# Performance work log

Measured on AMD Instinct MI355X. Metric: run time of the kernel, lower is better.

Reference implementation:

```python
import jax, jax.numpy as jnp
import numpy as np

B, IN_CHS, P = 512, 200, 19
CF, TF, K, D, NC = 64, 32, 48, 32, 16
BN_EPS = 1e-5


def _conv(x, w, b=None, dil=1):
    y = jax.lax.conv_general_dilated(x, w, (1, 1), 'VALID',
                                     rhs_dilation=(dil, dil),
                                     dimension_numbers=('NCHW', 'OIHW', 'NCHW'))
    if b is not None:
        y = y + b[None, :, None, None]
    return y


def _upsample_bilinear_ac(x, oh, ow):
    # bilinear with align_corners=True (torch UpsamplingBilinear2d)
    N, C, H, W = x.shape
    ys = jnp.linspace(0.0, H - 1.0, oh)
    xs = jnp.linspace(0.0, W - 1.0, ow)
    y0 = jnp.floor(ys).astype(jnp.int32)
    y1 = jnp.minimum(y0 + 1, H - 1)
    x0 = jnp.floor(xs).astype(jnp.int32)
    x1 = jnp.minimum(x0 + 1, W - 1)
    wy = (ys - y0.astype(ys.dtype))[None, None, :, None]
    wx = (xs - x0.astype(xs.dtype))[None, None, None, :]
    rows = x[:, :, y0, :] * (1.0 - wy) + x[:, :, y1, :] * wy
    return rows[:, :, :, x0] * (1.0 - wx) + rows[:, :, :, x1] * wx


def setup_inputs() -> dict:
    key = jax.random.key(0)
    ks = jax.random.split(key, 24)
    std1 = 1.0 / np.sqrt(K * D)
    inp = {
        'x': jax.random.normal(ks[0], (B, IN_CHS, P, P), jnp.float32),
        'w0': jax.random.normal(ks[1], (CF, IN_CHS, 3, 3), jnp.float32) * 0.02,
        'b0': jnp.zeros((CF,), jnp.float32),
        'w1': jax.random.normal(ks[2], (CF, CF, 3, 3), jnp.float32) * 0.05,
        'b1': jnp.zeros((CF,), jnp.float32),
        'w2': jax.random.normal(ks[3], (CF, CF, 3, 3), jnp.float32) * 0.05,
        'b2': jnp.zeros((CF,), jnp.float32),
        'wa': jax.random.normal(ks[4], (TF, CF, 1, 1), jnp.float32) * 0.08,
        'wb': jax.random.normal(ks[5], (TF, CF, 1, 1), jnp.float32) * 0.08,
        'wg': jax.random.normal(ks[6], (TF, CF, 1, 1), jnp.float32) * 0.08,
        'wd': jax.random.normal(ks[7], (CF, TF, 1, 1), jnp.float32) * 0.08,
        'wenc': jax.random.normal(ks[8], (D, CF, 1, 1), jnp.float32) * 0.08,
        'codewords': jax.random.uniform(ks[9], (K, D), jnp.float32, -std1, std1),
        'scale': jax.random.uniform(ks[10], (K,), jnp.float32, -1.0, 0.0),
        'w_att': jax.random.normal(ks[11], (CF, D), jnp.float32) * 0.1,
        'b_att': jnp.zeros((CF,), jnp.float32),
        'bn_g': jnp.ones((K,), jnp.float32),
        'bn_b': jnp.zeros((K,), jnp.float32),
        'w_d1': jax.random.normal(ks[12], (256, 3 * CF * P * P), jnp.float32) * 0.004,
        'b_d1': jnp.zeros((256,), jnp.float32),
        'w_d2': jax.random.normal(ks[13], (128, 256), jnp.float32) * 0.06,
        'b_d2': jnp.zeros((128,), jnp.float32),
        'w_d3': jax.random.normal(ks[14], (NC, 128), jnp.float32) * 0.09,
        'b_d3': jnp.zeros((NC,), jnp.float32),
    }
    return inp


def reference(x, w0, b0, w1, b1, w2, b2, wa, wb, wg, wd, wenc,
              codewords, scale, w_att, b_att, bn_g, bn_b,
              w_d1, b_d1, w_d2, b_d2, w_d3, b_d3):
    relu = jax.nn.relu
    Hin, Win = x.shape[2], x.shape[3]
    c1 = relu(_conv(x, w0, b0, 1))        # (b, CF, 17, 17)
    c2 = relu(_conv(c1, w1, b1, 2))       # (b, CF, 13, 13)
    xx = relu(_conv(c2, w2, b2, 3))       # (b, CF, 7, 7)
    n, c, h, w = xx.shape
    hw = h * w
    # non-local block; alpha view(n,-1,TF) is a RAW reshape in torch (not a transpose)
    alpha = _conv(xx, wa).reshape(n, hw, TF)
    beta = _conv(xx, wb).reshape(n, TF, hw)
    gam = relu(_conv(xx, wg)).reshape(n, TF, hw)
    ctx = jnp.matmul(alpha, beta)                 # (n, hw, hw)
    ctx = jax.nn.softmax(ctx, axis=0)             # torch F.softmax default dim for 3D tensor is 0
    ctx = jnp.matmul(gam, ctx).reshape(n, TF, h, w)
    ctx = _upsample_bilinear_ac(ctx, h, w)        # same-size -> identity, kept for fidelity
    xx = relu(_conv(ctx, wd)) + xx
    # soft VQ encoding
    Z = relu(_conv(xx, wenc)).reshape(n, D, hw).transpose(0, 2, 1)   # (b, hw, D)
    dist = scale * (jnp.sum(Z * Z, -1, keepdims=True)
                    + jnp.sum(codewords * codewords, -1)[None, None, :]
                    - 2.0 * jnp.einsum('bnd,kd->bnk', Z, codewords))  # (b, hw, K)
    A = jax.nn.softmax(dist, axis=2)
    # E[b,k,d] = sum_n A[b,n,k] * (Z[b,n,d] - C[k,d])
    E = jnp.einsum('bnk,bnd->bkd', A, Z) - A.sum(1)[:, :, None] * codewords[None]
    # BatchNorm1d(K) in training mode: stats over (batch, D) per code k
    mu = E.mean(axis=(0, 2), keepdims=True)
    var = E.var(axis=(0, 2), keepdims=True)
    En = relu((E - mu) / jnp.sqrt(var + BN_EPS) * bn_g[None, :, None] + bn_b[None, :, None])
    E_sum = En.sum(1)                              # (b, D)
    gate = jax.nn.sigmoid(E_sum @ w_att.T + b_att)  # (b, CF)
    xx = xx + xx * gate[:, :, None, None]
    ctx3 = _upsample_bilinear_ac(xx, Hin, Win)
    c2u = _upsample_bilinear_ac(c2, Hin, Win)
    c1u = _upsample_bilinear_ac(c1, Hin, Win)
    feat = jnp.concatenate((c1u, c2u, ctx3), axis=1).reshape(n, -1)  # (b, 69312)
    h1 = relu(feat @ w_d1.T + b_d1)
    h2 = relu(h1 @ w_d2.T + b_d2)
    return h2 @ w_d3.T + b_d3
```

## Files before the change

### kernel.cpp

```cpp
#include <hip/hip_runtime.h>
#include <math.h>


typedef __attribute__((ext_vector_type(8))) short short8v;
typedef __attribute__((ext_vector_type(4))) float f32x4;

#define OFF_WE1H  188928u
#define OFF_WE1L  2556416u
#define OFF_WE2H  4923904u
#define OFF_WE2L  6308352u
#define OFF_WE3H  7692800u
#define OFF_WE3L  8094208u
#define OFF_C1    8495616u
#define OFF_C2    17965568u
#define OFF_XX1   23503360u
#define OFF_ALPHA 25108992u
#define OFF_BETA  25911808u
#define OFF_GAM   26714624u
#define OFF_CTX   27517440u
#define OFF_CTX2  28746752u
#define OFF_XX2   29549568u
#define OFF_Z     31155200u
#define OFF_A     31958016u
#define OFF_E     33162240u
#define OFF_BNS   33948672u
#define OFF_XX3   33948768u
#define OFF_H1    35554400u
#define OFF_H2    35685472u

#define OFF_H1P   OFF_ALPHA

#define OFF_WH    OFF_ALPHA
#define OFF_WL    (OFF_ALPHA + 64512u)
#define OFF_W1H   (OFF_ALPHA + 129024u)
#define OFF_W1L   (OFF_W1H + 18432u)
#define OFF_W2H   (OFF_W1L + 18432u)
#define OFF_W2L   (OFF_W2H + 18432u)

__device__ __forceinline__ unsigned bf16_rne_bits(float v) {
    unsigned u = __float_as_uint(v);
    return (u + 0x7FFFu + ((u >> 16) & 1u)) >> 16;
}

__global__ __launch_bounds__(256) void sac_wsplit(const float* __restrict__ w0,
                                                  unsigned short* __restrict__ WH,
                                                  unsigned short* __restrict__ WL) {
    int idx = blockIdx.x * 256 + threadIdx.x;
    if (idx >= 129024) return;
    int ic = idx % 224;
    int c  = (idx / 224) % 64;
    int s  = idx / (224 * 64);
    int ky = s / 3, kx = s % 3;
    float v = 0.f;
    if (ic < 200) v = w0[((c * 200 + ic) * 3 + ky) * 3 + kx];
    unsigned hb = bf16_rne_bits(v);
    float hf = __uint_as_float(hb << 16);
    unsigned lb = bf16_rne_bits(v - hf);
    WH[idx] = (unsigned short)hb;
    WL[idx] = (unsigned short)lb;
}

__global__ __launch_bounds__(256) void sac_wsplit64(const float* __restrict__ wsrc,
                                                    unsigned short* __restrict__ WHo,
                                                    unsigned short* __restrict__ WLo) {
    int idx = blockIdx.x * 256 + threadIdx.x;
    if (idx >= 36864) return;
    int ic = idx & 63;
    int c  = (idx >> 6) & 63;
    int s  = idx >> 12;
    int ky = s / 3, kx = s - ky * 3;
    float v = wsrc[((c * 64 + ic) * 3 + ky) * 3 + kx];
    unsigned hb = bf16_rne_bits(v);
    float hf = __uint_as_float(hb << 16);
    unsigned lb = bf16_rne_bits(v - hf);
    WHo[idx] = (unsigned short)hb;
    WLo[idx] = (unsigned short)lb;
}

__global__ __launch_bounds__(256) void sac_upA(const float* __restrict__ w_d1,
                                               float* __restrict__ tmp, int S, int co) {
    int idx = blockIdx.x * 256 + threadIdx.x;
    int total = 256 * 64 * 19 * S;
    if (idx >= total) return;
    int xp = idx % S;
    int j  = (idx / S) % 19;
    int c  = (idx / (S * 19)) % 64;
    int o  = idx / (S * 19 * 64);
    const float* wrow = w_d1 + (size_t)o * 69312 + (size_t)(co + c) * 361 + j * 19;
    float ratio = (float)(S - 1) / 18.0f;
    float s = 0.f;
    for (int i = 0; i < 19; ++i) {
        float xs = i * ratio;
        int x0 = (int)floorf(xs);
        float wx = xs - (float)x0;
        int x1 = x0 + 1; if (x1 > S - 1) x1 = S - 1;
        float cf = (xp == x0 ? 1.f - wx : 0.f) + (xp == x1 ? wx : 0.f);
        s += cf * wrow[i];
    }
    tmp[idx] = s;
}
__global__ __launch_bounds__(256) void sac_upB_bf16(const float* __restrict__ tmp,
                                                    unsigned short* __restrict__ WEH,
                                                    unsigned short* __restrict__ WEL, int S) {
    int idx = blockIdx.x * 256 + threadIdx.x;
    int total = 256 * 64 * S * S;
    if (idx >= total) return;
    int xp = idx % S;
    int yp = (idx / S) % S;
    int c  = (idx / (S * S)) % 64;
    int o  = idx / (S * S * 64);
    const float* tp = tmp + (((size_t)o * 64 + c) * 19) * S + xp;
    float ratio = (float)(S - 1) / 18.0f;
    float s = 0.f;
    for (int j = 0; j < 19; ++j) {
        float ys = j * ratio;
        int y0 = (int)floorf(ys);
        float wy = ys - (float)y0;
        int y1 = y0 + 1; if (y1 > S - 1) y1 = S - 1;
        float cf = (yp == y0 ? 1.f - wy : 0.f) + (yp == y1 ? wy : 0.f);
        s += cf * tp[j * S];
    }
    unsigned hb = bf16_rne_bits(s);
    float hf = __uint_as_float(hb << 16);
    unsigned lb = bf16_rne_bits(s - hf);
    WEH[idx] = (unsigned short)hb;
    WEL[idx] = (unsigned short)lb;
}

template<int IW, int OW, int DIL, int TOTCH, int WSTR, int NMT, int NIRMAX>
__global__ __launch_bounds__(256, 4) void sac_convmfma(const float* __restrict__ x,
                                                       const unsigned short* __restrict__ WHp,
                                                       const unsigned short* __restrict__ WLp,
                                                       const float* __restrict__ bias,
                                                       float* __restrict__ out) {
    constexpr int OP = OW * OW;
    constexpr int ISZ = IW * IW;
    constexpr int NCHUNK = WSTR / 32;
    constexpr int NRC = NIRMAX * IW;
    __shared__ unsigned short XH[NRC * 32 + 64];
    __shared__ unsigned short XL[NRC * 32 + 64];
    int blk = blockIdx.x;
    int b = blk / NMT, mt = blk - b * NMT;
    int tid = threadIdx.x;
    int w = tid >> 6, l = tid & 63;
    int wm = w >> 1, wn = w & 1;
    int q = l >> 4, r = l & 15;
    int p_base = mt * 64 + wm * 32;
    int n_base = wn * 32;
    int pixA = p_base + r;      if (pixA > OP - 1) pixA = OP - 1;
    int pixB = p_base + 16 + r; if (pixB > OP - 1) pixB = OP - 1;
    int pyA = pixA / OW, pxa = pixA - pyA * OW;
    int pyB = pixB / OW, pxb = pixB - pyB * OW;
    int ir0 = (mt * 64) / OW;
    int rcA0 = (pyA - ir0) * IW + pxa;
    int rcB0 = (pyB - ir0) * IW + pxb;

    f32x4 acc[2][2];
    #pragma unroll
    for (int i = 0; i < 2; ++i)
        #pragma unroll
        for (int j = 0; j < 2; ++j) { acc[i][j].x = 0.f; acc[i][j].y = 0.f; acc[i][j].z = 0.f; acc[i][j].w = 0.f; }

    for (int cc = 0; cc < NCHUNK; ++cc) {
        int ch0 = cc * 32;
        __syncthreads();
        for (int f = tid; f < 8 * NRC; f += 256) {
            int chl4 = f / NRC, rc = f - chl4 * NRC;
            int ch = ch0 + chl4 * 4;
            int idx = ir0 * IW + rc; if (idx > ISZ - 1) idx = ISZ - 1;
            const float* gp = x + (size_t)b * (TOTCH * ISZ) + (size_t)ch * ISZ + idx;
            float v0 = (ch + 0 < TOTCH) ? gp[0] : 0.f;
            float v1 = (ch + 1 < TOTCH) ? gp[ISZ] : 0.f;
            float v2 = (ch + 2 < TOTCH) ? gp[2 * ISZ] : 0.f;
            float v3 = (ch + 3 < TOTCH) ? gp[3 * ISZ] : 0.f;
            unsigned h0 = bf16_rne_bits(v0); unsigned l0 = bf16_rne_bits(v0 - __uint_as_float(h0 << 16));
            unsigned h1 = bf16_rne_bits(v1); unsigned l1 = bf16_rne_bits(v1 - __uint_as_float(h1 << 16));
            unsigned h2 = bf16_rne_bits(v2); unsigned l2 = bf16_rne_bits(v2 - __uint_as_float(h2 << 16));
            unsigned h3 = bf16_rne_bits(v3); unsigned l3 = bf16_rne_bits(v3 - __uint_as_float(h3 << 16));
            unsigned bo = ((unsigned)(rc * 64 + chl4 * 8)) ^ (unsigned)((rc & 7) << 4);
            uint2 hv; hv.x = h0 | (h1 << 16); hv.y = h2 | (h3 << 16);
            uint2 lv; lv.x = l0 | (l1 << 16); lv.y = l2 | (l3 << 16);
            *(uint2*)((char*)XH + bo) = hv;
            *(uint2*)((char*)XL + bo) = lv;
        }
        __syncthreads();
        #pragma unroll 3
        for (int s9 = 0; s9 < 9; ++s9) {
            int ky = s9 / 3, kx = s9 - ky * 3;
            int rcA = rcA0 + DIL * (ky * IW + kx);
            int rcB = rcB0 + DIL * (ky * IW + kx);
            unsigned byA = ((unsigned)(rcA * 64 + q * 16)) ^ (unsigned)((rcA & 7) << 4);
            unsigned byB = ((unsigned)(rcB * 64 + q * 16)) ^ (unsigned)((rcB & 7) << 4);
            short8v ah0 = *(const short8v*)((const char*)XH + byA);
            short8v al0 = *(const short8v*)((const char*)XL + byA);
            short8v ah1 = *(const short8v*)((const char*)XH + byB);
            short8v al1 = *(const short8v*)((const char*)XL + byB);
            const unsigned short* pWH = WHp + (size_t)(s9 * 64 + n_base + r) * WSTR + ch0 + q * 8;
            const unsigned short* pWL = WLp + (size_t)(s9 * 64 + n_base + r) * WSTR + ch0 + q * 8;
            short8v bh0 = *(const short8v*)(pWH);
            short8v bh1 = *(const short8v*)(pWH + 16 * WSTR);
            short8v bl0 = *(const short8v*)(pWL);
            short8v bl1 = *(const short8v*)(pWL + 16 * WSTR);
            acc[0][0] = __builtin_amdgcn_mfma_f32_16x16x32_bf16(ah0, bh0, acc[0][0], 0, 0, 0);
            acc[0][1] = __builtin_amdgcn_mfma_f32_16x16x32_bf16(ah0, bh1, acc[0][1], 0, 0, 0);
            acc[1][0] = __builtin_amdgcn_mfma_f32_16x16x32_bf16(ah1, bh0, acc[1][0], 0, 0, 0);
            acc[1][1] = __builtin_amdgcn_mfma_f32_16x16x32_bf16(ah1, bh1, acc[1][1], 0, 0, 0);
            acc[0][0] = __builtin_amdgcn_mfma_f32_16x16x32_bf16(ah0, bl0, acc[0][0], 0, 0, 0);
            acc[0][1] = __builtin_amdgcn_mfma_f32_16x16x32_bf16(ah0, bl1, acc[0][1], 0, 0, 0);
            acc[1][0] = __builtin_amdgcn_mfma_f32_16x16x32_bf16(ah1, bl0, acc[1][0], 0, 0, 0);
            acc[1][1] = __builtin_amdgcn_mfma_f32_16x16x32_bf16(ah1, bl1, acc[1][1], 0, 0, 0);
            acc[0][0] = __builtin_amdgcn_mfma_f32_16x16x32_bf16(al0, bh0, acc[0][0], 0, 0, 0);
            acc[0][1] = __builtin_amdgcn_mfma_f32_16x16x32_bf16(al0, bh1, acc[0][1], 0, 0, 0);
            acc[1][0] = __builtin_amdgcn_mfma_f32_16x16x32_bf16(al1, bh0, acc[1][0], 0, 0, 0);
            acc[1][1] = __builtin_amdgcn_mfma_f32_16x16x32_bf16(al1, bh1, acc[1][1], 0, 0, 0);
        }
    }
    float bias0 = bias[n_base + r];
    float bias1 = bias[n_base + 16 + r];
    #pragma unroll
    for (int mf = 0; mf < 2; ++mf) {
        #pragma unroll
        for (int nf = 0; nf < 2; ++nf) {
            int ch = n_base + nf * 16 + r;
            float bs = nf ? bias1 : bias0;
            float* op = out + ((size_t)b * 64 + ch) * OP;
            #pragma unroll
            for (int j = 0; j < 4; ++j) {
                int pix = p_base + mf * 16 + q * 4 + j;
                if (pix < OP) {
                    float v = acc[mf][nf][j] + bs;
                    op[pix] = v > 0.f ? v : 0.f;
                }
            }
        }
    }
}

__global__ __launch_bounds__(256) void sac_abg(const float* __restrict__ xx1,
                                               const float* __restrict__ wa,
                                               const float* __restrict__ wb,
                                               const float* __restrict__ wg,
                                               float* __restrict__ alpha,
                                               float* __restrict__ beta,
                                               float* __restrict__ gam) {
    int b = blockIdx.x, tid = threadIdx.x;
    __shared__ float xsm[3136];
    __shared__ float ws3[3 * 2048];
    for (int f = tid; f < 3136; f += 256) xsm[f] = xx1[(size_t)b * 3136 + f];
    for (int f = tid; f < 2048; f += 256) {
        ws3[f] = wa[f]; ws3[2048 + f] = wb[f]; ws3[4096 + f] = wg[f];
    }
    __syncthreads();
    for (int f = tid; f < 4704; f += 256) {
        int which = f / 1568, r = f - which * 1568;
        int t = r / 49, p = r - t * 49;
        const float* w = &ws3[which * 2048 + t * 64];
        float s = 0.f;
        #pragma unroll 8
        for (int c = 0; c < 64; ++c) s += w[c] * xsm[c * 49 + p];
        if (which == 2) s = s > 0.f ? s : 0.f;
        float* o = (which == 0) ? alpha : (which == 1) ? beta : gam;
        o[(size_t)b * 1568 + r] = s;
    }
}

__global__ __launch_bounds__(256) void sac_ctx(const float* __restrict__ alpha,
                                               const float* __restrict__ beta,
                                               float* __restrict__ ctx) {
    int b = blockIdx.x, tid = threadIdx.x;
    __shared__ float af[1568];
    __shared__ float bt[1568];
    for (int f = tid; f < 1568; f += 256) {
        af[f] = alpha[(size_t)b * 1568 + f];
        bt[f] = beta[(size_t)b * 1568 + f];
    }
    __syncthreads();
    for (int f = tid; f < 2401; f += 256) {
        int i = f / 49, l = f - i * 49;
        float s = 0.f;
        #pragma unroll 8
        for (int j = 0; j < 32; ++j) s += af[i * 32 + j] * bt[j * 49 + l];
        ctx[(size_t)b * 2401 + f] = s;
    }
}

__global__ __launch_bounds__(256) void sac_softmax0(float* __restrict__ ctx) {
    int pos = blockIdx.x;
    int tid = threadIdx.x;
    float v0 = ctx[(size_t)tid * 2401 + pos];
    float v1 = ctx[(size_t)(tid + 256) * 2401 + pos];
    float m = fmaxf(v0, v1);
    #pragma unroll
    for (int off = 32; off > 0; off >>= 1) m = fmaxf(m, __shfl_xor(m, off, 64));
    __shared__ float sred[4];
    __shared__ float ssum[4];
    int lane = tid & 63, wid = tid >> 6;
    if (lane == 0) sred[wid] = m;
    __syncthreads();
    m = fmaxf(fmaxf(sred[0], sred[1]), fmaxf(sred[2], sred[3]));
    float e0 = expf(v0 - m), e1 = expf(v1 - m);
    float s = e0 + e1;
    #pragma unroll
    for (int off = 32; off > 0; off >>= 1) s += __shfl_xor(s, off, 64);
    if (lane == 0) ssum[wid] = s;
    __syncthreads();
    float inv = 1.f / (ssum[0] + ssum[1] + ssum[2] + ssum[3]);
    ctx[(size_t)tid * 2401 + pos] = e0 * inv;
    ctx[(size_t)(tid + 256) * 2401 + pos] = e1 * inv;
}

__global__ __launch_bounds__(256) void sac_ctx2(const float* __restrict__ gam,
                                                const float* __restrict__ ctx,
                                                float* __restrict__ ctx2) {
    int b = blockIdx.x, tid = threadIdx.x;
    __shared__ float gs[1568];
    __shared__ float cs[2401];
    for (int f = tid; f < 1568; f += 256) gs[f] = gam[(size_t)b * 1568 + f];
    for (int f = tid; f < 2401; f += 256) cs[f] = ctx[(size_t)b * 2401 + f];
    __syncthreads();
    for (int f = tid; f < 1568; f += 256) {
        int t = f / 49, l = f - t * 49;
        float s = 0.f;
        #pragma unroll 7
        for (int i = 0; i < 49; ++i) s += gs[t * 49 + i] * cs[i * 49 + l];
        ctx2[(size_t)b * 1568 + f] = s;
    }
}

__global__ __launch_bounds__(256) void sac_xx2(const float* __restrict__ ctx2,
                                               const float* __restrict__ wd,
                                               const float* __restrict__ xx1,
                                               float* __restrict__ xx2) {
    int b = blockIdx.x, tid = threadIdx.x;
    __shared__ float cs[1568];
    __shared__ float wds[2048];
    for (int f = tid; f < 1568; f += 256) cs[f] = ctx2[(size_t)b * 1568 + f];
    for (int f = tid; f < 2048; f += 256) wds[f] = wd[f];
    __syncthreads();
    for (int f = tid; f < 3136; f += 256) {
        int c = f / 49, p = f - c * 49;
        float s = 0.f;
        #pragma unroll 8
        for (int t = 0; t < 32; ++t) s += wds[c * 32 + t] * cs[t * 49 + p];
        s = s > 0.f ? s : 0.f;
        xx2[(size_t)b * 3136 + f] = s + xx1[(size_t)b * 3136 + f];
    }
}

__global__ __launch_bounds__(256) void sac_z(const float* __restrict__ xx2,
                                             const float* __restrict__ wenc,
                                             float* __restrict__ Z) {
    int b = blockIdx.x, tid = threadIdx.x;
    __shared__ float xsm[3136];
    __shared__ float wt[2048];
    for (int f = tid; f < 3136; f += 256) xsm[f] = xx2[(size_t)b * 3136 + f];
    for (int f = tid; f < 2048; f += 256) { int d = f >> 6, c = f & 63; wt[c * 32 + d] = wenc[f]; }
    __syncthreads();
    for (int f = tid; f < 1568; f += 256) {
        int p = f >> 5, d = f & 31;
        float s = 0.f;
        #pragma unroll 8
        for (int c = 0; c < 64; ++c) s += wt[c * 32 + d] * xsm[c * 49 + p];
        Z[(size_t)b * 1568 + f] = s > 0.f ? s : 0.f;
    }
}

__global__ __launch_bounds__(256) void sac_dist(const float* __restrict__ Z,
                                                const float* __restrict__ cw,
                                                const float* __restrict__ scale,
                                                float* __restrict__ A) {
    __shared__ float cws[1536];
    __shared__ float c2s[48];
    __shared__ float scs[48];
    int tid = threadIdx.x;
    for (int f = tid; f < 1536; f += 256) cws[f] = cw[f];
    if (tid < 48) scs[tid] = scale[tid];
    __syncthreads();
    if (tid < 48) {
        float s = 0.f;
        for (int d = 0; d < 32; ++d) { float v = cws[tid * 32 + d]; s += v * v; }
        c2s[tid] = s;
    }
    __syncthreads();
    int idx = blockIdx.x * 256 + tid;
    if (idx >= 25088) return;
    const float4* zp = (const float4*)(Z + (size_t)idx * 32);
    float zr[32];
    #pragma unroll
    for (int q = 0; q < 8; ++q) {
        float4 v = zp[q];
        zr[q * 4] = v.x; zr[q * 4 + 1] = v.y; zr[q * 4 + 2] = v.z; zr[q * 4 + 3] = v.w;
    }
    float z2 = 0.f;
    #pragma unroll
    for (int d = 0; d < 32; ++d) z2 += zr[d] * zr[d];
    float* ap = A + (size_t)idx * 48;
    for (int k = 0; k < 48; ++k) {
        float dot = 0.f;
        #pragma unroll
        for (int d = 0; d < 32; ++d) dot += zr[d] * cws[k * 32 + d];
        ap[k] = scs[k] * (z2 + c2s[k] - 2.f * dot);
    }
}

__global__ __launch_bounds__(256) void sac_asoft(float* __restrict__ A) {
    int idx = blockIdx.x * 256 + threadIdx.x;
    if (idx >= 25088) return;
    float* ap = A + (size_t)idx * 48;
    float v[48];
    float m = -1e30f;
    #pragma unroll
    for (int k = 0; k < 48; ++k) { v[k] = ap[k]; m = fmaxf(m, v[k]); }
    float s = 0.f;
    #pragma unroll
    for (int k = 0; k < 48; ++k) { v[k] = expf(v[k] - m); s += v[k]; }
    float inv = 1.f / s;
    #pragma unroll
    for (int k = 0; k < 48; ++k) ap[k] = v[k] * inv;
}

__global__ __launch_bounds__(256) void sac_e(const float* __restrict__ A,
                                             const float* __restrict__ Z,
                                             const float* __restrict__ cw,
                                             float* __restrict__ E) {
    int b = blockIdx.x, tid = threadIdx.x;
    __shared__ float As[2352];
    __shared__ float Zs[1568];
    __shared__ float asum[48];
    for (int f = tid; f < 2352; f += 256) As[f] = A[(size_t)b * 2352 + f];
    for (int f = tid; f < 1568; f += 256) Zs[f] = Z[(size_t)b * 1568 + f];
    __syncthreads();
    if (tid < 48) {
        float s = 0.f;
        for (int p = 0; p < 49; ++p) s += As[p * 48 + tid];
        asum[tid] = s;
    }
    __syncthreads();
    for (int f = tid; f < 1536; f += 256) {
        int k = f >> 5, d = f & 31;
        float s = 0.f;
        #pragma unroll 7
        for (int p = 0; p < 49; ++p) s += As[p * 48 + k] * Zs[p * 32 + d];
        E[(size_t)b * 1536 + f] = s - asum[k] * cw[f];
    }
}

__global__ __launch_bounds__(256) void sac_bnstat(const float* __restrict__ E,
                                                  float* __restrict__ bns) {
    int k = blockIdx.x, tid = threadIdx.x;
    __shared__ float sr[4];
    float s = 0.f;
    for (int i = tid; i < 16384; i += 256) {
        int b = i >> 5, d = i & 31;
        s += E[((size_t)b * 48 + k) * 32 + d];
    }
    #pragma unroll
    for (int off = 32; off > 0; off >>= 1) s += __shfl_xor(s, off, 64);
    int lane = tid & 63, wid = tid >> 6;
    if (lane == 0) sr[wid] = s;
    __syncthreads();
    float mu = (sr[0] + sr[1] + sr[2] + sr[3]) / 16384.f;
    float q = 0.f;
    for (int i = tid; i < 16384; i += 256) {
        int b = i >> 5, d = i & 31;
        float v = E[((size_t)b * 48 + k) * 32 + d] - mu;
        q += v * v;
    }
    #pragma unroll
    for (int off = 32; off > 0; off >>= 1) q += __shfl_xor(q, off, 64);
    __syncthreads();
    if (lane == 0) sr[wid] = q;
    __syncthreads();
    if (tid == 0) {
        float var = (sr[0] + sr[1] + sr[2] + sr[3]) / 16384.f;
        bns[k] = mu;
        bns[48 + k] = rsqrtf(var + 1e-5f);
    }
}

__global__ __launch_bounds__(256) void sac_gate(const float* __restrict__ E,
                                                const float* __restrict__ bns,
                                                const float* __restrict__ bn_g,
                                                const float* __restrict__ bn_b,
                                                const float* __restrict__ w_att,
                                                const float* __restrict__ b_att,
                                                const float* __restrict__ xx2,
                                                float* __restrict__ xx3) {
    int b = blockIdx.x, tid = threadIdx.x;
    __shared__ float esd[32];
    __shared__ float gs[64];
    if (tid < 32) {
        int d = tid;
        float s = 0.f;
        for (int k = 0; k < 48; ++k) {
            float v = (E[((size_t)b * 48 + k) * 32 + d] - bns[k]) * bns[48 + k] * bn_g[k] + bn_b[k];
            s += v > 0.f ? v : 0.f;
        }
        esd[d] = s;
    }
    __syncthreads();
    if (tid < 64) {
        int c = tid;
        float a = b_att[c];
        #pragma unroll 8
        for (int d = 0; d < 32; ++d) a += esd[d] * w_att[c * 32 + d];
        gs[c] = 1.f / (1.f + expf(-a)) + 1.f;
    }
    __syncthreads();
    for (int f = tid; f < 3136; f += 256) {
        int c = f / 49;
        xx3[(size_t)b * 3136 + f] = xx2[(size_t)b * 3136 + f] * gs[c];
    }
}

__global__ __launch_bounds__(256, 4) void sac_d1gemm_mfma(const float* __restrict__ c1,
                                                          const float* __restrict__ c2,
                                                          const float* __restrict__ xx3,
                                                          const unsigned short* __restrict__ we1h,
                                                          const unsigned short* __restrict__ we1l,
                                                          const unsigned short* __restrict__ we2h,
                                                          const unsigned short* __restrict__ we2l,
                                                          const unsigned short* __restrict__ we3h,
                                                          const unsigned short* __restrict__ we3l,
                                                          float* __restrict__ h1p) {
    constexpr int KCH = 128;
    __shared__ unsigned short AH[64 * KCH + 64];
    __shared__ unsigned short AL[64 * KCH + 64];
    int blk = blockIdx.x;
    int g = blk >> 5, r5 = blk & 31;
    int b0 = (r5 >> 2) * 64, o0 = (r5 & 3) * 64;
    const float* Ab; const unsigned short *WHb, *WLb; int astr, klen, kbase;
    if (g < 16)      { int slab = g >> 2, kq4 = g & 3;
                       Ab = c1;  WHb = we1h; WLb = we1l; astr = 18496; klen = 1156; kbase = slab * 4624 + kq4 * 1156; }
    else if (g < 24) { int gg = g - 16; int slab = gg >> 2, kq4 = gg & 3;
                       Ab = c2;  WHb = we2h; WLb = we2l; astr = 10816; klen = 1352; kbase = slab * 5408 + kq4 * 1352; }
    else             { int kq4 = g - 24;
                       Ab = xx3; WHb = we3h; WLb = we3l; astr = 3136;  klen = 784;  kbase = kq4 * 784; }
    int tid = threadIdx.x;
    int w = tid >> 6, l = tid & 63;
    int wm = w >> 1, wn = w & 1;
    int q = l >> 4, r = l & 15;

    f32x4 acc[2][2];
    #pragma unroll
    for (int i = 0; i < 2; ++i)
        #pragma unroll
        for (int j = 0; j < 2; ++j) { acc[i][j].x = 0.f; acc[i][j].y = 0.f; acc[i][j].z = 0.f; acc[i][j].w = 0.f; }

    int nkch = (klen + KCH - 1) / KCH;
    for (int kc = 0; kc < nkch; ++kc) {
        int k0 = kc * KCH;
        __syncthreads();
        for (int f = tid; f < 64 * (KCH / 2); f += 256) {
            int row = f >> 6, col2 = (f & 63) << 1;
            int kk = k0 + col2;
            float va = 0.f, vb = 0.f;
            if (kk < klen) {
                float2 v = *(const float2*)(Ab + (size_t)(b0 + row) * astr + kbase + kk);
                va = v.x; vb = v.y;
            }
            unsigned h0 = bf16_rne_bits(va); unsigned l0 = bf16_rne_bits(va - __uint_as_float(h0 << 16));
            unsigned h1 = bf16_rne_bits(vb); unsigned l1 = bf16_rne_bits(vb - __uint_as_float(h1 << 16));
            unsigned bo = ((unsigned)(row * 256 + col2 * 2)) ^ (unsigned)((row & 7) << 4);
            *(unsigned*)((char*)AH + bo) = h0 | (h1 << 16);
            *(unsigned*)((char*)AL + bo) = l0 | (l1 << 16);
        }
        __syncthreads();
        #pragma unroll
        for (int ks = 0; ks < KCH / 32; ++ks) {
            int k = ks * 32 + q * 8;
            int rowA0 = wm * 32 + r, rowA1 = wm * 32 + 16 + r;
            unsigned byA0 = ((unsigned)(rowA0 * 256 + k * 2)) ^ (unsigned)((rowA0 & 7) << 4);
            unsigned byA1 = ((unsigned)(rowA1 * 256 + k * 2)) ^ (unsigned)((rowA1 & 7) << 4);
            short8v ah0 = *(const short8v*)((const char*)AH + byA0);
            short8v al0 = *(const short8v*)((const char*)AL + byA0);
            short8v ah1 = *(const short8v*)((const char*)AH + byA1);
            short8v al1 = *(const short8v*)((const char*)AL + byA1);
            size_t wofs = (size_t)(o0 + wn * 32 + r) * astr + kbase + k0 + k;
            short8v bh0 = *(const short8v*)(WHb + wofs);
            short8v bh1 = *(const short8v*)(WHb + wofs + (size_t)16 * astr);
            short8v bl0 = *(const short8v*)(WLb + wofs);
            short8v bl1 = *(const short8v*)(WLb + wofs + (size_t)16 * astr);
            acc[0][0] = __builtin_amdgcn_mfma_f32_16x16x32_bf16(ah0, bh0, acc[0][0], 0, 0, 0);
            acc[0][1] = __builtin_amdgcn_mfma_f32_16x16x32_bf16(ah0, bh1, acc[0][1], 0, 0, 0);
            acc[1][0] = __builtin_amdgcn_mfma_f32_16x16x32_bf16(ah1, bh0, acc[1][0], 0, 0, 0);
            acc[1][1] = __builtin_amdgcn_mfma_f32_16x16x32_bf16(ah1, bh1, acc[1][1], 0, 0, 0);
            acc[0][0] = __builtin_amdgcn_mfma_f32_16x16x32_bf16(ah0, bl0, acc[0][0], 0, 0, 0);
            acc[0][1] = __builtin_amdgcn_mfma_f32_16x16x32_bf16(ah0, bl1, acc[0][1], 0, 0, 0);
            acc[1][0] = __builtin_amdgcn_mfma_f32_16x16x32_bf16(ah1, bl0, acc[1][0], 0, 0, 0);
            acc[1][1] = __builtin_amdgcn_mfma_f32_16x16x32_bf16(ah1, bl1, acc[1][1], 0, 0, 0);
            acc[0][0] = __builtin_amdgcn_mfma_f32_16x16x32_bf16(al0, bh0, acc[0][0], 0, 0, 0);
            acc[0][1] = __builtin_amdgcn_mfma_f32_16x16x32_bf16(al0, bh1, acc[0][1], 0, 0, 0);
            acc[1][0] = __builtin_amdgcn_mfma_f32_16x16x32_bf16(al1, bh0, acc[1][0], 0, 0, 0);
            acc[1][1] = __builtin_amdgcn_mfma_f32_16x16x32_bf16(al1, bh1, acc[1][1], 0, 0, 0);
        }
    }
    #pragma unroll
    for (int mf = 0; mf < 2; ++mf) {
        #pragma unroll
        for (int nf = 0; nf < 2; ++nf) {
            int o = o0 + wn * 32 + nf * 16 + r;
            #pragma unroll
            for (int j = 0; j < 4; ++j) {
                int batch = b0 + wm * 32 + mf * 16 + q * 4 + j;
                h1p[((size_t)g * 512 + batch) * 256 + o] = acc[mf][nf][j];
            }
        }
    }
}

__global__ __launch_bounds__(256) void sac_h1red(const float* __restrict__ h1p,
                                                 const float* __restrict__ b_d1,
                                                 float* __restrict__ h1) {
    int i = blockIdx.x * 256 + threadIdx.x;
    int o = i & 255;
    float s = b_d1[o];
    #pragma unroll
    for (int t = 0; t < 28; ++t) s += h1p[(size_t)t * 131072 + i];
    h1[i] = s > 0.f ? s : 0.f;
}

__global__ __launch_bounds__(256) void sac_h2(const float* __restrict__ h1,
                                              const float* __restrict__ w_d2,
                                              const float* __restrict__ b_d2,
                                              float* __restrict__ h2) {
    int idx = blockIdx.x * 256 + threadIdx.x;
    int b = idx >> 7, o = idx & 127;
    const float* hp = h1 + b * 256;
    const float* wp = w_d2 + o * 256;
    float s = b_d2[o];
    #pragma unroll 4
    for (int k = 0; k < 256; ++k) s += hp[k] * wp[k];
    h2[idx] = s > 0.f ? s : 0.f;
}

__global__ __launch_bounds__(256) void sac_out(const float* __restrict__ h2,
                                               const float* __restrict__ w_d3,
                                               const float* __restrict__ b_d3,
                                               float* __restrict__ out) {
    int idx = blockIdx.x * 256 + threadIdx.x;
    int b = idx >> 4, j = idx & 15;
    const float* hp = h2 + b * 128;
    const float* wp = w_d3 + j * 128;
    float s = b_d3[j];
    #pragma unroll 4
    for (int k = 0; k < 128; ++k) s += hp[k] * wp[k];
    out[idx] = s;
}

extern "C" void kernel_launch(void* const* d_in, const int* in_sizes, int n_in,
                              void* d_out, int out_size, void* d_ws, size_t ws_size,
                              hipStream_t stream) {
    (void)in_sizes; (void)n_in; (void)out_size; (void)ws_size;
    const float* x     = (const float*)d_in[0];
    const float* w0    = (const float*)d_in[1];
    const float* b0    = (const float*)d_in[2];
    const float* w1    = (const float*)d_in[3];
    const float* b1    = (const float*)d_in[4];
    const float* w2    = (const float*)d_in[5];
    const float* b2    = (const float*)d_in[6];
    const float* wa    = (const float*)d_in[7];
    const float* wb    = (const float*)d_in[8];
    const float* wg    = (const float*)d_in[9];
    const float* wd    = (const float*)d_in[10];
    const float* wenc  = (const float*)d_in[11];
    const float* cw    = (const float*)d_in[12];
    const float* scale = (const float*)d_in[13];
    const float* w_att = (const float*)d_in[14];
    const float* b_att = (const float*)d_in[15];
    const float* bn_g  = (const float*)d_in[16];
    const float* bn_b  = (const float*)d_in[17];
    const float* w_d1  = (const float*)d_in[18];
    const float* b_d1  = (const float*)d_in[19];
    const float* w_d2  = (const float*)d_in[20];
    const float* b_d2  = (const float*)d_in[21];
    const float* w_d3  = (const float*)d_in[22];
    const float* b_d3  = (const float*)d_in[23];

    float* ws    = (float*)d_ws;
    unsigned short* WE1H = (unsigned short*)(ws + OFF_WE1H);
    unsigned short* WE1L = (unsigned short*)(ws + OFF_WE1L);
    unsigned short* WE2H = (unsigned short*)(ws + OFF_WE2H);
    unsigned short* WE2L = (unsigned short*)(ws + OFF_WE2L);
    unsigned short* WE3H = (unsigned short*)(ws + OFF_WE3H);
    unsigned short* WE3L = (unsigned short*)(ws + OFF_WE3L);
    float* TMP   = ws + OFF_C1;
    float* C1    = ws + OFF_C1;
    float* C2    = ws + OFF_C2;
    float* XX1   = ws + OFF_XX1;
    float* ALPHA = ws + OFF_ALPHA;
    float* BETA  = ws + OFF_BETA;
    float* GAM   = ws + OFF_GAM;
    float* CTX   = ws + OFF_CTX;
    float* H1P   = ws + OFF_H1P;
    float* CTX2  = ws + OFF_CTX2;
    float* XX2   = ws + OFF_XX2;
    float* Z     = ws + OFF_Z;
    float* A     = ws + OFF_A;
    float* E     = ws + OFF_E;
    float* BNS   = ws + OFF_BNS;
    float* XX3   = ws + OFF_XX3;
    float* H1    = ws + OFF_H1;
    float* H2    = ws + OFF_H2;
    unsigned short* WH  = (unsigned short*)(ws + OFF_WH);
    unsigned short* WL  = (unsigned short*)(ws + OFF_WL);
    unsigned short* W1H = (unsigned short*)(ws + OFF_W1H);
    unsigned short* W1L = (unsigned short*)(ws + OFF_W1L);
    unsigned short* W2H = (unsigned short*)(ws + OFF_W2H);
    unsigned short* W2L = (unsigned short*)(ws + OFF_W2L);

    sac_wsplit<<<504, 256, 0, stream>>>(w0, WH, WL);
    sac_wsplit64<<<144, 256, 0, stream>>>(w1, W1H, W1L);
    sac_wsplit64<<<144, 256, 0, stream>>>(w2, W2H, W2L);

    sac_upA<<<20672, 256, 0, stream>>>(w_d1, TMP, 17, 0);
    sac_upB_bf16<<<18496, 256, 0, stream>>>(TMP, WE1H, WE1L, 17);
    sac_upA<<<15808, 256, 0, stream>>>(w_d1, TMP, 13, 64);
    sac_upB_bf16<<<10816, 256, 0, stream>>>(TMP, WE2H, WE2L, 13);
    sac_upA<<<8512, 256, 0, stream>>>(w_d1, TMP, 7, 128);
    sac_upB_bf16<<<3136, 256, 0, stream>>>(TMP, WE3H, WE3L, 7);

    sac_convmfma<19, 17, 1, 200, 224, 5, 7 ><<<2560, 256, 0, stream>>>(x,  WH,  WL,  b0, C1);
    sac_convmfma<17, 13, 2,  64,  64, 3, 10><<<1536, 256, 0, stream>>>(C1, W1H, W1L, b1, C2);
    sac_convmfma<13,  7, 3,  64,  64, 1, 13><<< 512, 256, 0, stream>>>(C2, W2H, W2L, b2, XX1);

    sac_abg<<<512, 256, 0, stream>>>(XX1, wa, wb, wg, ALPHA, BETA, GAM);
    sac_ctx<<<512, 256, 0, stream>>>(ALPHA, BETA, CTX);
    sac_softmax0<<<2401, 256, 0, stream>>>(CTX);
    sac_ctx2<<<512, 256, 0, stream>>>(GAM, CTX, CTX2);
    sac_xx2<<<512, 256, 0, stream>>>(CTX2, wd, XX1, XX2);

    sac_z<<<512, 256, 0, stream>>>(XX2, wenc, Z);
    sac_dist<<<98, 256, 0, stream>>>(Z, cw, scale, A);
    sac_asoft<<<98, 256, 0, stream>>>(A);
    sac_e<<<512, 256, 0, stream>>>(A, Z, cw, E);
    sac_bnstat<<<48, 256, 0, stream>>>(E, BNS);
    sac_gate<<<512, 256, 0, stream>>>(E, BNS, bn_g, bn_b, w_att, b_att, XX2, XX3);

    sac_d1gemm_mfma<<<896, 256, 0, stream>>>(C1, C2, XX3, WE1H, WE1L, WE2H, WE2L, WE3H, WE3L, H1P);
    sac_h1red<<<512, 256, 0, stream>>>(H1P, b_d1, H1);
    sac_h2<<<256, 256, 0, stream>>>(H1, w_d2, b_d2, H2);
    sac_out<<<32, 256, 0, stream>>>(H2, w_d3, b_d3, (float*)d_out);
}
```

Before: 864.6 us.

## Interleave conv weight hi/lo, pad LDS rows, split batch softmax into stats

The conv weights are now stored as one interleaved hi/lo bf16 array per 32-channel chunk and tap, so each MFMA step reads contiguous weight vectors. The input tile in LDS moves from an XOR swizzle to an 80-byte padded row stride, with a wave-per-row-block staging loop and precomputed LDS pointers. The batch-axis softmax no longer rewrites CTX in place: a small stats kernel computes a per-position max and inverse sum, and the ctx2 kernel applies the normalisation while it loads. The stats kernel launches only 38 blocks of 64 threads, each thread making two serial strided passes over 512 batches, which risks low occupancy.

```diff
diff --git a/kernel.cpp b/kernel.cpp
--- a/kernel.cpp
+++ b/kernel.cpp
@@ -29,52 +29,51 @@
 #define OFF_H2    35685472u
 
 #define OFF_H1P   OFF_ALPHA
-
-#define OFF_WH    OFF_ALPHA
-#define OFF_WL    (OFF_ALPHA + 64512u)
-#define OFF_W1H   (OFF_ALPHA + 129024u)
-#define OFF_W1L   (OFF_W1H + 18432u)
-#define OFF_W2H   (OFF_W1L + 18432u)
-#define OFF_W2L   (OFF_W2H + 18432u)
+#define OFF_MS    OFF_BETA
+
+#define OFF_WHL0  OFF_ALPHA
+#define OFF_W1HL  (OFF_ALPHA + 129024u)
+#define OFF_W2HL  (OFF_W1HL + 36864u)
 
 __device__ __forceinline__ unsigned bf16_rne_bits(float v) {
     unsigned u = __float_as_uint(v);
     return (u + 0x7FFFu + ((u >> 16) & 1u)) >> 16;
 }
 
-__global__ __launch_bounds__(256) void sac_wsplit(const float* __restrict__ w0,
-                                                  unsigned short* __restrict__ WH,
-                                                  unsigned short* __restrict__ WL) {
+__global__ __launch_bounds__(256) void sac_wsplit_c0(const float* __restrict__ w0,
+                                                     unsigned short* __restrict__ WHL) {
     int idx = blockIdx.x * 256 + threadIdx.x;
-    if (idx >= 129024) return;
-    int ic = idx % 224;
-    int c  = (idx / 224) % 64;
-    int s  = idx / (224 * 64);
+    if (idx >= 258048) return;
+    int t = idx & 63;
+    int c = (idx >> 6) & 63;
+    int rem = idx >> 12;
+    int s = rem % 9, cc = rem / 9;
+    int ch = cc * 32 + (t & 31);
     int ky = s / 3, kx = s % 3;
-    float v = 0.f;
-    if (ic < 200) v = w0[((c * 200 + ic) * 3 + ky) * 3 + kx];
+    float v = (ch < 200) ? w0[((c * 200 + ch) * 3 + ky) * 3 + kx] : 0.f;
     unsigned hb = bf16_rne_bits(v);
-    float hf = __uint_as_float(hb << 16);
-    unsigned lb = bf16_rne_bits(v - hf);
-    WH[idx] = (unsigned short)hb;
-    WL[idx] = (unsigned short)lb;
-}
-
-__global__ __launch_bounds__(256) void sac_wsplit64(const float* __restrict__ wsrc,
-                                                    unsigned short* __restrict__ WHo,
-                                                    unsigned short* __restrict__ WLo) {
+    unsigned short o;
+    if (t < 32) o = (unsigned short)hb;
+    else        o = (unsigned short)bf16_rne_bits(v - __uint_as_float(hb << 16));
+    WHL[idx] = o;
+}
+
+__global__ __launch_bounds__(256) void sac_wsplit_c12(const float* __restrict__ w,
+                                                      unsigned short* __restrict__ WHL) {
     int idx = blockIdx.x * 256 + threadIdx.x;
-    if (idx >= 36864) return;
-    int ic = idx & 63;
-    int c  = (idx >> 6) & 63;
-    int s  = idx >> 12;
-    int ky = s / 3, kx = s - ky * 3;
-    float v = wsrc[((c * 64 + ic) * 3 + ky) * 3 + kx];
+    if (idx >= 73728) return;
+    int t = idx & 63;
+    int c = (idx >> 6) & 63;
+    int rem = idx >> 12;
+    int s = rem % 9, cc = rem / 9;
+    int ch = cc * 32 + (t & 31);
+    int ky = s / 3, kx = s % 3;
+    float v = w[((c * 64 + ch) * 3 + ky) * 3 + kx];
     unsigned hb = bf16_rne_bits(v);
-    float hf = __uint_as_float(hb << 16);
-    unsigned lb = bf16_rne_bits(v - hf);
-    WHo[idx] = (unsigned short)hb;
-    WLo[idx] = (unsigned short)lb;
+    unsigned short o;
+    if (t < 32) o = (unsigned short)hb;
+    else        o = (unsigned short)bf16_rne_bits(v - __uint_as_float(hb << 16));
+    WHL[idx] = o;
 }
 
 __global__ __launch_bounds__(256) void sac_upA(const float* __restrict__ w_d1,
@@ -127,23 +126,23 @@
     WEL[idx] = (unsigned short)lb;
 }
 
-template<int IW, int OW, int DIL, int TOTCH, int WSTR, int NMT, int NIRMAX>
+template<int IW, int OW, int DIL, int TOTCH, int NCHUNK, int NMT, int NIRMAX>
 __global__ __launch_bounds__(256, 4) void sac_convmfma(const float* __restrict__ x,
-                                                       const unsigned short* __restrict__ WHp,
-                                                       const unsigned short* __restrict__ WLp,
+                                                       const unsigned short* __restrict__ WHL,
                                                        const float* __restrict__ bias,
                                                        float* __restrict__ out) {
     constexpr int OP = OW * OW;
     constexpr int ISZ = IW * IW;
-    constexpr int NCHUNK = WSTR / 32;
     constexpr int NRC = NIRMAX * IW;
-    __shared__ unsigned short XH[NRC * 32 + 64];
-    __shared__ unsigned short XL[NRC * 32 + 64];
+    constexpr int RB = (NRC + 31) / 32;
+    __shared__ __align__(16) unsigned short XH[NRC * 40];
+    __shared__ __align__(16) unsigned short XL[NRC * 40];
     int blk = blockIdx.x;
     int b = blk / NMT, mt = blk - b * NMT;
     int tid = threadIdx.x;
-    int w = tid >> 6, l = tid & 63;
-    int wm = w >> 1, wn = w & 1;
+    int wv = tid >> 6, l = tid & 63;
+    int lh = l >> 5, li = l & 31;
+    int wm = wv >> 1, wn = wv & 1;
     int q = l >> 4, r = l & 15;
     int p_base = mt * 64 + wm * 32;
     int n_base = wn * 32;
@@ -154,6 +153,10 @@
     int ir0 = (mt * 64) / OW;
     int rcA0 = (pyA - ir0) * IW + pxa;
     int rcB0 = (pyB - ir0) * IW + pxb;
+    const char* pXAH = (const char*)XH + rcA0 * 80 + q * 16;
+    const char* pXAL = (const char*)XL + rcA0 * 80 + q * 16;
+    const char* pXBH = (const char*)XH + rcB0 * 80 + q * 16;
+    const char* pXBL = (const char*)XL + rcB0 * 80 + q * 16;
 
     f32x4 acc[2][2];
     #pragma unroll
@@ -162,45 +165,44 @@
         for (int j = 0; j < 2; ++j) { acc[i][j].x = 0.f; acc[i][j].y = 0.f; acc[i][j].z = 0.f; acc[i][j].w = 0.f; }
 
     for (int cc = 0; cc < NCHUNK; ++cc) {
-        int ch0 = cc * 32;
         __syncthreads();
-        for (int f = tid; f < 8 * NRC; f += 256) {
-            int chl4 = f / NRC, rc = f - chl4 * NRC;
-            int ch = ch0 + chl4 * 4;
-            int idx = ir0 * IW + rc; if (idx > ISZ - 1) idx = ISZ - 1;
-            const float* gp = x + (size_t)b * (TOTCH * ISZ) + (size_t)ch * ISZ + idx;
-            float v0 = (ch + 0 < TOTCH) ? gp[0] : 0.f;
-            float v1 = (ch + 1 < TOTCH) ? gp[ISZ] : 0.f;
-            float v2 = (ch + 2 < TOTCH) ? gp[2 * ISZ] : 0.f;
-            float v3 = (ch + 3 < TOTCH) ? gp[3 * ISZ] : 0.f;
-            unsigned h0 = bf16_rne_bits(v0); unsigned l0 = bf16_rne_bits(v0 - __uint_as_float(h0 << 16));
-            unsigned h1 = bf16_rne_bits(v1); unsigned l1 = bf16_rne_bits(v1 - __uint_as_float(h1 << 16));
-            unsigned h2 = bf16_rne_bits(v2); unsigned l2 = bf16_rne_bits(v2 - __uint_as_float(h2 << 16));
-            unsigned h3 = bf16_rne_bits(v3); unsigned l3 = bf16_rne_bits(v3 - __uint_as_float(h3 << 16));
-            unsigned bo = ((unsigned)(rc * 64 + chl4 * 8)) ^ (unsigned)((rc & 7) << 4);
-            uint2 hv; hv.x = h0 | (h1 << 16); hv.y = h2 | (h3 << 16);
-            uint2 lv; lv.x = l0 | (l1 << 16); lv.y = l2 | (l3 << 16);
-            *(uint2*)((char*)XH + bo) = hv;
-            *(uint2*)((char*)XL + bo) = lv;
+        for (int it = wv; it < 4 * RB; it += 4) {
+            int cg = it / RB, rb = it - cg * RB;
+            int rc = rb * 32 + li;
+            if (rc < NRC) {
+                int chl4 = cg * 2 + lh;
+                int ch = cc * 32 + chl4 * 4;
+                int idx = ir0 * IW + rc; if (idx > ISZ - 1) idx = ISZ - 1;
+                const float* gp = x + (size_t)b * (TOTCH * ISZ) + (size_t)ch * ISZ + idx;
+                float v0 = (ch + 0 < TOTCH) ? gp[0] : 0.f;
+                float v1 = (ch + 1 < TOTCH) ? gp[ISZ] : 0.f;
+                float v2 = (ch + 2 < TOTCH) ? gp[2 * ISZ] : 0.f;
+                float v3 = (ch + 3 < TOTCH) ? gp[3 * ISZ] : 0.f;
+                unsigned h0 = bf16_rne_bits(v0); unsigned l0 = bf16_rne_bits(v0 - __uint_as_float(h0 << 16));
+                unsigned h1 = bf16_rne_bits(v1); unsigned l1 = bf16_rne_bits(v1 - __uint_as_float(h1 << 16));
+                unsigned h2 = bf16_rne_bits(v2); unsigned l2 = bf16_rne_bits(v2 - __uint_as_float(h2 << 16));
+                unsigned h3 = bf16_rne_bits(v3); unsigned l3 = bf16_rne_bits(v3 - __uint_as_float(h3 << 16));
+                unsigned bo = (unsigned)(rc * 80 + chl4 * 8);
+                uint2 hv; hv.x = h0 | (h1 << 16); hv.y = h2 | (h3 << 16);
+                uint2 lv; lv.x = l0 | (l1 << 16); lv.y = l2 | (l3 << 16);
+                *(uint2*)((char*)XH + bo) = hv;
+                *(uint2*)((char*)XL + bo) = lv;
+            }
         }
         __syncthreads();
-        #pragma unroll 3
+        const unsigned short* Wc = WHL + ((size_t)(cc * 9) * 64 + n_base + r) * 64 + q * 8;
+        #pragma unroll
         for (int s9 = 0; s9 < 9; ++s9) {
-            int ky = s9 / 3, kx = s9 - ky * 3;
-            int rcA = rcA0 + DIL * (ky * IW + kx);
-            int rcB = rcB0 + DIL * (ky * IW + kx);
-            unsigned byA = ((unsigned)(rcA * 64 + q * 16)) ^ (unsigned)((rcA & 7) << 4);
-            unsigned byB = ((unsigned)(rcB * 64 + q * 16)) ^ (unsigned)((rcB & 7) << 4);
-            short8v ah0 = *(const short8v*)((const char*)XH + byA);
-            short8v al0 = *(const short8v*)((const char*)XL + byA);
-            short8v ah1 = *(const short8v*)((const char*)XH + byB);
-            short8v al1 = *(const short8v*)((const char*)XL + byB);
-            const unsigned short* pWH = WHp + (size_t)(s9 * 64 + n_base + r) * WSTR + ch0 + q * 8;
-            const unsigned short* pWL = WLp + (size_t)(s9 * 64 + n_base + r) * WSTR + ch0 + q * 8;
-            short8v bh0 = *(const short8v*)(pWH);
-            short8v bh1 = *(const short8v*)(pWH + 16 * WSTR);
-            short8v bl0 = *(const short8v*)(pWL);
-            short8v bl1 = *(const short8v*)(pWL + 16 * WSTR);
+            const int D = DIL * ((s9 / 3) * IW + (s9 % 3)) * 80;
+            short8v ah0 = *(const short8v*)(pXAH + D);
+            short8v al0 = *(const short8v*)(pXAL + D);
+            short8v ah1 = *(const short8v*)(pXBH + D);
+            short8v al1 = *(const short8v*)(pXBL + D);
+            const unsigned short* Wt = Wc + s9 * 4096;
+            short8v bh0 = *(const short8v*)(Wt);
+            short8v bl0 = *(const short8v*)(Wt + 32);
+            short8v bh1 = *(const short8v*)(Wt + 1024);
+            short8v bl1 = *(const short8v*)(Wt + 1056);
             acc[0][0] = __builtin_amdgcn_mfma_f32_16x16x32_bf16(ah0, bh0, acc[0][0], 0, 0, 0);
             acc[0][1] = __builtin_amdgcn_mfma_f32_16x16x32_bf16(ah0, bh1, acc[0][1], 0, 0, 0);
             acc[1][0] = __builtin_amdgcn_mfma_f32_16x16x32_bf16(ah1, bh0, acc[1][0], 0, 0, 0);
@@ -284,39 +286,28 @@
     }
 }
 
-__global__ __launch_bounds__(256) void sac_softmax0(float* __restrict__ ctx) {
-    int pos = blockIdx.x;
-    int tid = threadIdx.x;
-    float v0 = ctx[(size_t)tid * 2401 + pos];
-    float v1 = ctx[(size_t)(tid + 256) * 2401 + pos];
-    float m = fmaxf(v0, v1);
-    #pragma unroll
-    for (int off = 32; off > 0; off >>= 1) m = fmaxf(m, __shfl_xor(m, off, 64));
-    __shared__ float sred[4];
-    __shared__ float ssum[4];
-    int lane = tid & 63, wid = tid >> 6;
-    if (lane == 0) sred[wid] = m;
-    __syncthreads();
-    m = fmaxf(fmaxf(sred[0], sred[1]), fmaxf(sred[2], sred[3]));
-    float e0 = expf(v0 - m), e1 = expf(v1 - m);
-    float s = e0 + e1;
-    #pragma unroll
-    for (int off = 32; off > 0; off >>= 1) s += __shfl_xor(s, off, 64);
-    if (lane == 0) ssum[wid] = s;
-    __syncthreads();
-    float inv = 1.f / (ssum[0] + ssum[1] + ssum[2] + ssum[3]);
-    ctx[(size_t)tid * 2401 + pos] = e0 * inv;
-    ctx[(size_t)(tid + 256) * 2401 + pos] = e1 * inv;
+__global__ __launch_bounds__(64) void sac_smstat(const float* __restrict__ ctx,
+                                                 float* __restrict__ ms) {
+    int pos = blockIdx.x * 64 + threadIdx.x;
+    if (pos >= 2401) return;
+    float m = -1e30f;
+    for (int b = 0; b < 512; ++b) m = fmaxf(m, ctx[(size_t)b * 2401 + pos]);
+    float s = 0.f;
+    for (int b = 0; b < 512; ++b) s += expf(ctx[(size_t)b * 2401 + pos] - m);
+    ms[pos] = m;
+    ms[2401 + pos] = 1.f / s;
 }
 
 __global__ __launch_bounds__(256) void sac_ctx2(const float* __restrict__ gam,
                                                 const float* __restrict__ ctx,
+                                                const float* __restrict__ ms,
                                                 float* __restrict__ ctx2) {
     int b = blockIdx.x, tid = threadIdx.x;
     __shared__ float gs[1568];
     __shared__ float cs[2401];
     for (int f = tid; f < 1568; f += 256) gs[f] = gam[(size_t)b * 1568 + f];
-    for (int f = tid; f < 2401; f += 256) cs[f] = ctx[(size_t)b * 2401 + f];
+    for (int f = tid; f < 2401; f += 256)
+        cs[f] = expf(ctx[(size_t)b * 2401 + f] - ms[f]) * ms[2401 + f];
     __syncthreads();
     for (int f = tid; f < 1568; f += 256) {
         int t = f / 49, l = f - t * 49;
@@ -702,16 +693,14 @@
     float* XX3   = ws + OFF_XX3;
     float* H1    = ws + OFF_H1;
     float* H2    = ws + OFF_H2;
-    unsigned short* WH  = (unsigned short*)(ws + OFF_WH);
-    unsigned short* WL  = (unsigned short*)(ws + OFF_WL);
-    unsigned short* W1H = (unsigned short*)(ws + OFF_W1H);
-    unsigned short* W1L = (unsigned short*)(ws + OFF_W1L);
-    unsigned short* W2H = (unsigned short*)(ws + OFF_W2H);
-    unsigned short* W2L = (unsigned short*)(ws + OFF_W2L);
-
-    sac_wsplit<<<504, 256, 0, stream>>>(w0, WH, WL);
-    sac_wsplit64<<<144, 256, 0, stream>>>(w1, W1H, W1L);
-    sac_wsplit64<<<144, 256, 0, stream>>>(w2, W2H, W2L);
+    float* MS    = ws + OFF_MS;
+    unsigned short* WHL0 = (unsigned short*)(ws + OFF_WHL0);
+    unsigned short* W1HL = (unsigned short*)(ws + OFF_W1HL);
+    unsigned short* W2HL = (unsigned short*)(ws + OFF_W2HL);
+
+    sac_wsplit_c0<<<1008, 256, 0, stream>>>(w0, WHL0);
+    sac_wsplit_c12<<<288, 256, 0, stream>>>(w1, W1HL);
+    sac_wsplit_c12<<<288, 256, 0, stream>>>(w2, W2HL);
 
     sac_upA<<<20672, 256, 0, stream>>>(w_d1, TMP, 17, 0);
     sac_upB_bf16<<<18496, 256, 0, stream>>>(TMP, WE1H, WE1L, 17);
@@ -720,14 +709,14 @@
     sac_upA<<<8512, 256, 0, stream>>>(w_d1, TMP, 7, 128);
     sac_upB_bf16<<<3136, 256, 0, stream>>>(TMP, WE3H, WE3L, 7);
 
-    sac_convmfma<19, 17, 1, 200, 224, 5, 7 ><<<2560, 256, 0, stream>>>(x,  WH,  WL,  b0, C1);
-    sac_convmfma<17, 13, 2,  64,  64, 3, 10><<<1536, 256, 0, stream>>>(C1, W1H, W1L, b1, C2);
-    sac_convmfma<13,  7, 3,  64,  64, 1, 13><<< 512, 256, 0, stream>>>(C2, W2H, W2L, b2, XX1);
+    sac_convmfma<19, 17, 1, 200, 7, 5, 7 ><<<2560, 256, 0, stream>>>(x,  WHL0, b0, C1);
+    sac_convmfma<17, 13, 2,  64, 2, 3, 10><<<1536, 256, 0, stream>>>(C1, W1HL, b1, C2);
+    sac_convmfma<13,  7, 3,  64, 2, 1, 13><<< 512, 256, 0, stream>>>(C2, W2HL, b2, XX1);
 
     sac_abg<<<512, 256, 0, stream>>>(XX1, wa, wb, wg, ALPHA, BETA, GAM);
     sac_ctx<<<512, 256, 0, stream>>>(ALPHA, BETA, CTX);
-    sac_softmax0<<<2401, 256, 0, stream>>>(CTX);
-    sac_ctx2<<<512, 256, 0, stream>>>(GAM, CTX, CTX2);
+    sac_smstat<<<38, 64, 0, stream>>>(CTX, MS);
+    sac_ctx2<<<512, 256, 0, stream>>>(GAM, CTX, MS, CTX2);
     sac_xx2<<<512, 256, 0, stream>>>(CTX2, wd, XX1, XX2);
 
     sac_z<<<512, 256, 0, stream>>>(XX2, wenc, Z);
```

Result: slower. 1.054 ms (+21.9%).
